# Performance work log

Hardware: AMD Instinct MI355X
Metric: run time of the kernel (lower is better)

The kernel has to match this reference:

```python
import jax, jax.numpy as jnp
import numpy as np

B, T, D = 8, 1024, 1024

def setup_inputs() -> dict:
    key = jax.random.key(0)
    ks = jax.random.split(key, 9)
    s = D ** -0.5
    return {
        "x": jax.random.normal(ks[0], (B, T, D), dtype=jnp.float32),
        "w_q": jax.random.normal(ks[1], (D, D), dtype=jnp.float32) * s,
        "b_q": jax.random.normal(ks[2], (D,), dtype=jnp.float32) * 0.02,
        "w_k": jax.random.normal(ks[3], (D, D), dtype=jnp.float32) * s,
        "b_k": jax.random.normal(ks[4], (D,), dtype=jnp.float32) * 0.02,
        "w_v": jax.random.normal(ks[5], (D, D), dtype=jnp.float32) * s,
        "b_v": jax.random.normal(ks[6], (D,), dtype=jnp.float32) * 0.02,
        "w_o": jax.random.normal(ks[7], (D, D), dtype=jnp.float32) * s,
        "b_o": jax.random.normal(ks[8], (D,), dtype=jnp.float32) * 0.02,
    }

def reference(x, w_q, b_q, w_k, b_k, w_v, b_v, w_o, b_o):
    d = x.shape[-1]
    scale = jnp.asarray(d, x.dtype) ** -0.5
    q = jnp.einsum('btd,ed->bte', x, w_q) + b_q  # nn.Linear: x @ W^T + b
    k = jnp.einsum('btd,ed->bte', x, w_k) + b_k
    v = jnp.einsum('btd,ed->bte', x, w_v) + b_v
    t = x.shape[1]
    causal = jnp.tril(jnp.ones((t, t), dtype=bool))  # (T, T)
    scores = jnp.einsum('bqd,bkd->bqk', q, k) * scale
    scores = jnp.where(causal, scores, -jnp.inf)
    attn = jax.nn.softmax(scores, axis=-1)  # max-subtraction folded in
    out = jnp.einsum('bqk,bkd->bqd', attn, v)
    return jnp.einsum('btd,ed->bte', out, w_o) + b_o
```

## Files before the change

### kernel.cpp

```cpp
#include <hip/hip_runtime.h>

typedef unsigned short u16;
typedef __attribute__((ext_vector_type(8))) short short8;
typedef __attribute__((ext_vector_type(4))) float f32x4;


__device__ __forceinline__ u16 f2bf(float f) {
  unsigned u = __builtin_bit_cast(unsigned, f);
  u += 0x7fffu + ((u >> 16) & 1u);
  return (u16)(u >> 16);
}

__device__ __forceinline__ void gload16(const void* g, void* l) {
  __builtin_amdgcn_global_load_lds(
      (const __attribute__((address_space(1))) unsigned*)g,
      (__attribute__((address_space(3))) unsigned*)l, 16, 0, 0);
}


#define PTILE(RB_C, RB_N, DOSTAGE, VM, LAST)                                  \
  {                                                                           \
    char* cA = sA0 + cur * 49152;                                             \
                                                       \
    if (DOSTAGE) {                                                            \
      const int ns = (cur + 2 >= 3) ? cur - 1 : cur + 2;                      \
      char* dA = sA0 + ns * 49152;                                            \
      _Pragma("unroll") for (int j = 0; j < 3; ++j) {                         \
        gload16(ga[j], dA + la[j]); ga[j] += 64; }                            \
    }                                                                         \
    _Pragma("unroll") for (int kk = 0; kk < 2; ++kk)                          \
      _Pragma("unroll") for (int i = 0; i < 2; ++i) {                         \
        const int rm = wr + 32 + i * 16 + l16;                                \
        a1f[kk][i] = *(const short8*)(cA + rm * 128 +                         \
            (((kk << 2) + quad) ^ (rm & 7)) * 16);                            \
      }                                                                       \
    asm volatile("s_waitcnt lgkmcnt(4)" ::: "memory");                        \
    __builtin_amdgcn_sched_barrier(0);                                        \
    __builtin_amdgcn_s_setprio(1);                                            \
    _Pragma("unroll") for (int kk = 0; kk < 2; ++kk)                          \
      _Pragma("unroll") for (int i = 0; i < 2; ++i)                           \
        _Pragma("unroll") for (int j = 0; j < 4; ++j)                         \
          acc[i][j] = __builtin_amdgcn_mfma_f32_16x16x32_bf16(                \
              a0f[kk][i], RB_C[kk][j], acc[i][j], 0, 0, 0);                   \
    __builtin_amdgcn_s_setprio(0);                                            \
                                                       \
    if (DOSTAGE) {                                                            \
      const int ns = (cur + 2 >= 3) ? cur - 1 : cur + 2;                      \
      char* dA = sA0 + ns * 49152; char* dB = dA + 32768;                     \
      gload16(ga[3], dA + la[3]); ga[3] += 64;                                \
      _Pragma("unroll") for (int j = 0; j < 2; ++j) {                         \
        gload16(gb[j], dB + lb[j]); gb[j] += 64; }                            \
    }                                                                         \
    if (!(LAST)) {                                                            \
      asm volatile("s_waitcnt vmcnt(" #VM ") lgkmcnt(0)" ::: "memory");       \
      __builtin_amdgcn_s_barrier();                                           \
      asm volatile("" ::: "memory");                                          \
      const int nc = (cur + 1 >= 3) ? 0 : cur + 1;                            \
      char* nA = sA0 + nc * 49152; char* nB = nA + 32768;                     \
      _Pragma("unroll") for (int kk = 0; kk < 2; ++kk)                        \
        _Pragma("unroll") for (int j = 0; j < 4; ++j) {                       \
          const int rn = wc + j * 16 + l16;                                   \
          RB_N[kk][j] = *(const short8*)(nB + rn * 128 +                      \
              (((kk << 2) + quad) ^ (rn & 7)) * 16);                          \
        }                                                                     \
      _Pragma("unroll") for (int kk = 0; kk < 2; ++kk)                        \
        _Pragma("unroll") for (int i = 0; i < 2; ++i) {                       \
          const int rm = wr + i * 16 + l16;                                   \
          a0f[kk][i] = *(const short8*)(nA + rm * 128 +                       \
              (((kk << 2) + quad) ^ (rm & 7)) * 16);                          \
        }                                                                     \
    } else {                                                                  \
      asm volatile("s_waitcnt lgkmcnt(0)" ::: "memory");                      \
    }                                                                         \
    __builtin_amdgcn_sched_barrier(0);                                        \
    __builtin_amdgcn_s_setprio(1);                                            \
    _Pragma("unroll") for (int kk = 0; kk < 2; ++kk)                          \
      _Pragma("unroll") for (int i = 0; i < 2; ++i)                           \
        _Pragma("unroll") for (int j = 0; j < 4; ++j)                         \
          acc[2 + i][j] = __builtin_amdgcn_mfma_f32_16x16x32_bf16(            \
              a1f[kk][i], RB_C[kk][j], acc[2 + i][j], 0, 0, 0);               \
    __builtin_amdgcn_s_setprio(0);                                            \
    cur = (cur + 1 >= 3) ? 0 : cur + 1;                                       \
  }

__device__ __forceinline__ void gemm_256x128(
    const u16* __restrict__ A, const u16* __restrict__ B,
    int m0, int n0, int ntiles, char* smem, f32x4 acc[4][4])
{
  const int tid  = threadIdx.x;
  const int lane = tid & 63;
  const int quad = lane >> 4;
  const int l16  = lane & 15;
  const int wave = tid >> 6;
  const int wr   = (wave >> 1) << 6;
  const int wc   = (wave & 1) << 6;

  const u16* ga[4]; int la[4];
  const u16* gb[2]; int lb[2];
#pragma unroll
  for (int j = 0; j < 4; ++j) {
    const int L = j * 512 + tid;
    const int r = L >> 3;
    const int c = (L & 7) ^ (r & 7);
    la[j] = L * 16;
    ga[j] = A + (size_t)(m0 + r) * 1024 + c * 8;
  }
#pragma unroll
  for (int j = 0; j < 2; ++j) {
    const int L = j * 512 + tid;
    const int r = L >> 3;
    const int c = (L & 7) ^ (r & 7);
    lb[j] = L * 16;
    gb[j] = B + (size_t)(n0 + r) * 1024 + c * 8;
  }
  char* const sA0 = smem;

  short8 bfr0[2][4], bfr1[2][4];
  short8 a0f[2][2], a1f[2][2];

  {
    char* dA = sA0; char* dB = sA0 + 32768;
#pragma unroll
    for (int j = 0; j < 4; ++j) { gload16(ga[j], dA + la[j]); ga[j] += 64; }
#pragma unroll
    for (int j = 0; j < 2; ++j) { gload16(gb[j], dB + lb[j]); gb[j] += 64; }
    dA = sA0 + 49152; dB = dA + 32768;
#pragma unroll
    for (int j = 0; j < 4; ++j) { gload16(ga[j], dA + la[j]); ga[j] += 64; }
#pragma unroll
    for (int j = 0; j < 2; ++j) { gload16(gb[j], dB + lb[j]); gb[j] += 64; }
  }
  asm volatile("s_waitcnt vmcnt(6)" ::: "memory");
  __builtin_amdgcn_s_barrier();
  asm volatile("" ::: "memory");
  {
    char* nA = sA0; char* nB = sA0 + 32768;
#pragma unroll
    for (int kk = 0; kk < 2; ++kk)
#pragma unroll
      for (int j = 0; j < 4; ++j) {
        const int rn = wc + j * 16 + l16;
        bfr0[kk][j] = *(const short8*)(nB + rn * 128 + (((kk << 2) + quad) ^ (rn & 7)) * 16);
      }
#pragma unroll
    for (int kk = 0; kk < 2; ++kk)
#pragma unroll
      for (int i = 0; i < 2; ++i) {
        const int rm = wr + i * 16 + l16;
        a0f[kk][i] = *(const short8*)(nA + rm * 128 + (((kk << 2) + quad) ^ (rm & 7)) * 16);
      }
  }

  int cur = 0;
  const int npair = (ntiles >> 1) - 1;
#pragma unroll 1
  for (int it = 0; it < npair; ++it) {
    PTILE(bfr0, bfr1, true, 6, false);
    PTILE(bfr1, bfr0, true, 6, false);
  }
  PTILE(bfr0, bfr1, false, 0, false);
  PTILE(bfr1, bfr0, false, 0, true);
  __syncthreads();
}

#define ACC_ZERO4(acc) { _Pragma("unroll") for (int i=0;i<4;++i) \
  _Pragma("unroll") for (int j=0;j<4;++j) \
  _Pragma("unroll") for (int r=0;r<4;++r) acc[i][j][r]=0.f; }

__device__ __forceinline__ void store256x128_bf16(
    f32x4 acc[4][4], const float* bias, int n0,
    u16* C, int m0, char* smem)
{
  const int tid = threadIdx.x, lane = tid & 63, wave = tid >> 6;
  const int quad = lane >> 4, l16 = lane & 15;
  const int wr = (wave >> 1) << 6, wc = (wave & 1) << 6;
  u16* t = (u16*)smem;
#pragma unroll
  for (int j = 0; j < 4; ++j) {
    const int nn = wc + j * 16 + l16;
    const float bj = bias[n0 + nn];
#pragma unroll
    for (int i = 0; i < 4; ++i) {
      const int mm = wr + i * 16 + quad * 4;
#pragma unroll
      for (int r = 0; r < 4; ++r)
        t[(mm + r) * 136 + nn] = f2bf(acc[i][j][r] + bj);
    }
  }
  __syncthreads();
#pragma unroll
  for (int it = 0; it < 8; ++it) {
    const int L = it * 512 + tid;
    const int mm = L >> 4, cc = L & 15;
    *(uint4*)(C + (size_t)(m0 + mm) * 1024 + n0 + cc * 8) =
        *(const uint4*)(t + mm * 136 + cc * 8);
  }
}

__global__ __launch_bounds__(256) void cast_inputs(
    const float* __restrict__ x,  const float* __restrict__ wq,
    const float* __restrict__ wk, const float* __restrict__ wv,
    const float* __restrict__ wo,
    u16* xb, u16* wqb, u16* wkb, u16* wvb, u16* wob, float* rsum)
{
  int b = blockIdx.x;
  if (b < 8) {
    float4 z = {0.f, 0.f, 0.f, 0.f};
    *(float4*)(rsum + (b * 256 + threadIdx.x) * 4) = z;
  }
  const float* src; u16* dst; int base;
  if (b < 4096) { src = x; dst = xb; base = b * 2048; }
  else {
    int r = (b - 4096) >> 9, bb = (b - 4096) & 511;
    base = bb * 2048;
    src = (r == 0) ? wq : (r == 1) ? wk : (r == 2) ? wv : wo;
    dst = (r == 0) ? wqb : (r == 1) ? wkb : (r == 2) ? wvb : wob;
  }
  int i0 = base + threadIdx.x * 8;
  float4 f0 = *(const float4*)(src + i0);
  float4 f1 = *(const float4*)(src + i0 + 4);
  short8 o;
  o[0]=(short)f2bf(f0.x); o[1]=(short)f2bf(f0.y); o[2]=(short)f2bf(f0.z); o[3]=(short)f2bf(f0.w);
  o[4]=(short)f2bf(f1.x); o[5]=(short)f2bf(f1.y); o[6]=(short)f2bf(f1.z); o[7]=(short)f2bf(f1.w);
  *(short8*)(dst + i0) = o;
}

__global__ __launch_bounds__(512, 2) void proj_qkv(
    const u16* __restrict__ xb,
    const u16* __restrict__ wqb, const u16* __restrict__ wkb, const u16* __restrict__ wvb,
    const float* __restrict__ bq, const float* __restrict__ bk, const float* __restrict__ bv,
    u16* q, u16* k, u16* vt)
{
  __shared__ char smem[147456];
  const int z = blockIdx.y;
  const u16* W = (z == 0) ? wqb : (z == 1) ? wkb : wvb;
  const float* bias = (z == 0) ? bq : (z == 1) ? bk : bv;
  const int id = blockIdx.x;
  const int m0 = ((id & 7) * 4 + ((id >> 3) & 3)) * 256;
  const int n0 = (id >> 5) * 128;

  f32x4 acc[4][4]; ACC_ZERO4(acc);
  gemm_256x128(xb, W, m0, n0, 16, smem, acc);

  if (z < 2) {
    store256x128_bf16(acc, bias, n0, (z == 0) ? q : k, m0, smem);
  } else {
    const int tid = threadIdx.x, lane = tid & 63, wave = tid >> 6;
    const int quad = lane >> 4, l16 = lane & 15;
    const int wr = (wave >> 1) << 6, wc = (wave & 1) << 6;
    u16* t = (u16*)smem;
#pragma unroll
    for (int j = 0; j < 4; ++j) {
      const int nn = wc + j * 16 + l16;
      const float bj = bias[n0 + nn];
#pragma unroll
      for (int i = 0; i < 4; ++i) {
        const int mm = wr + i * 16 + quad * 4;
#pragma unroll
        for (int r = 0; r < 4; ++r)
          t[nn * 264 + mm + r] = f2bf(acc[i][j][r] + bj);
      }
    }
    __syncthreads();
    const int b = m0 >> 10, t0 = m0 & 1023;
#pragma unroll
    for (int it = 0; it < 8; ++it) {
      const int L = it * 512 + tid;
      const int nn = L >> 5, cc = L & 31;
      *(uint4*)(vt + ((size_t)b << 20) + (size_t)(n0 + nn) * 1024 + t0 + cc * 8) =
          *(const uint4*)(t + nn * 264 + cc * 8);
    }
  }
}

__global__ __launch_bounds__(512, 2) void qk_exp256(
    const u16* __restrict__ q, const u16* __restrict__ k,
    u16* __restrict__ probs, float* __restrict__ rowsum)
{
  __shared__ char smem[147456];
  const int id = blockIdx.x;
  const int b = id / 20;
  const int t = id - b * 20;
  const int qi = (t < 2) ? 0 : (t < 6) ? 1 : (t < 12) ? 2 : 3;
  const int pre = (qi == 0) ? 0 : (qi == 1) ? 2 : (qi == 2) ? 6 : 12;
  const int kt = t - pre;
  const int m0 = qi * 256, n0 = kt * 128;
  const u16* A = q + ((size_t)b << 20);
  const u16* B = k + ((size_t)b << 20);

  f32x4 acc[4][4]; ACC_ZERO4(acc);
  gemm_256x128(A, B, m0, n0, 16, smem, acc);

  const int tid = threadIdx.x, lane = tid & 63, wave = tid >> 6;
  const int quad = lane >> 4, l16 = lane & 15;
  const int wr = (wave >> 1) << 6, wc = (wave & 1) << 6;

  float part[4][4];
#pragma unroll
  for (int i = 0; i < 4; ++i)
#pragma unroll
    for (int r = 0; r < 4; ++r) part[i][r] = 0.f;

  u16* tl = (u16*)smem;
#pragma unroll
  for (int j = 0; j < 4; ++j) {
    const int nn = wc + j * 16 + l16;
#pragma unroll
    for (int i = 0; i < 4; ++i) {
      const int mm = wr + i * 16 + quad * 4;
#pragma unroll
      for (int r = 0; r < 4; ++r) {
        float e = __expf(acc[i][j][r] * 0.03125f);
        if ((n0 + nn) > (m0 + mm + r)) e = 0.f;
        part[i][r] += e;
        tl[(mm + r) * 136 + nn] = f2bf(e);
      }
    }
  }
  float* rs = rowsum + b * 1024 + m0;
#pragma unroll
  for (int i = 0; i < 4; ++i)
#pragma unroll
    for (int r = 0; r < 4; ++r) {
      float v = part[i][r];
      v += __shfl_xor(v, 1); v += __shfl_xor(v, 2);
      v += __shfl_xor(v, 4); v += __shfl_xor(v, 8);
      if (l16 == 0) atomicAdd(rs + wr + i * 16 + quad * 4 + r, v);
    }
  __syncthreads();
  u16* C = probs + ((size_t)b << 20);
#pragma unroll
  for (int it = 0; it < 8; ++it) {
    const int L = it * 512 + tid;
    const int mm = L >> 4, cc = L & 15;
    *(uint4*)(C + (size_t)(m0 + mm) * 1024 + n0 + cc * 8) =
        *(const uint4*)(tl + mm * 136 + cc * 8);
  }
}

__global__ __launch_bounds__(512, 2) void pv256(
    const u16* __restrict__ probs, const u16* __restrict__ vt,
    const float* __restrict__ rowsum, u16* __restrict__ o)
{
  __shared__ char smem[147456];
  const int id = blockIdx.x;
  const int b = id & 7;
  const int u = id >> 3;
  const int qi = 3 - (u & 3);
  const int nb = u >> 2;
  const int m0 = qi * 256, n0 = nb * 128;
  const int nt = (qi + 1) * 4;
  const u16* A = probs + ((size_t)b << 20);
  const u16* B = vt + ((size_t)b << 20);

  f32x4 acc[4][4]; ACC_ZERO4(acc);
  gemm_256x128(A, B, m0, n0, nt, smem, acc);

  const int tid = threadIdx.x, lane = tid & 63, wave = tid >> 6;
  const int quad = lane >> 4, l16 = lane & 15;
  const int wr = (wave >> 1) << 6, wc = (wave & 1) << 6;
  const float* rs = rowsum + b * 1024 + m0;
  u16* tl = (u16*)smem;
#pragma unroll
  for (int i = 0; i < 4; ++i)
#pragma unroll
    for (int r = 0; r < 4; ++r) {
      const int mm = wr + i * 16 + quad * 4 + r;
      const float inv = 1.0f / rs[mm];
#pragma unroll
      for (int j = 0; j < 4; ++j)
        tl[mm * 136 + wc + j * 16 + l16] = f2bf(acc[i][j][r] * inv);
    }
  __syncthreads();
  u16* C = o + ((size_t)b << 20);
#pragma unroll
  for (int it = 0; it < 8; ++it) {
    const int L = it * 512 + tid;
    const int mm = L >> 4, cc = L & 15;
    *(uint4*)(C + (size_t)(m0 + mm) * 1024 + n0 + cc * 8) =
        *(const uint4*)(tl + mm * 136 + cc * 8);
  }
}

__global__ __launch_bounds__(512, 2) void proj_o(
    const u16* __restrict__ ob, const u16* __restrict__ wob,
    const float* __restrict__ bo, float* __restrict__ out)
{
  __shared__ char smem[147456];
  const int id = blockIdx.x;
  const int m0 = ((id & 7) * 4 + ((id >> 3) & 3)) * 256;
  const int n0 = (id >> 5) * 128;
  f32x4 acc[4][4]; ACC_ZERO4(acc);
  gemm_256x128(ob, wob, m0, n0, 16, smem, acc);

  const int tid = threadIdx.x, lane = tid & 63, wave = tid >> 6;
  const int quad = lane >> 4, l16 = lane & 15;
  const int wr = (wave >> 1) << 6, wc = (wave & 1) << 6;
  float* tf = (float*)smem;
#pragma unroll
  for (int j = 0; j < 4; ++j) {
    const int nn = wc + j * 16 + l16;
    const float bj = bo[n0 + nn];
#pragma unroll
    for (int i = 0; i < 4; ++i)
#pragma unroll
      for (int r = 0; r < 4; ++r)
        tf[(wr + i * 16 + quad * 4 + r) * 132 + nn] = acc[i][j][r] + bj;
  }
  __syncthreads();
#pragma unroll
  for (int it = 0; it < 16; ++it) {
    const int L = it * 512 + tid;
    const int mm = L >> 5, cc = L & 31;
    *(float4*)(out + (size_t)(m0 + mm) * 1024 + n0 + cc * 4) =
        *(const float4*)(tf + mm * 132 + cc * 4);
  }
}

extern "C" void kernel_launch(void* const* d_in, const int* in_sizes, int n_in,
                              void* d_out, int out_size, void* d_ws, size_t ws_size,
                              hipStream_t stream) {
  const float* x  = (const float*)d_in[0];
  const float* wq = (const float*)d_in[1];
  const float* bq = (const float*)d_in[2];
  const float* wk = (const float*)d_in[3];
  const float* bk = (const float*)d_in[4];
  const float* wv = (const float*)d_in[5];
  const float* bv = (const float*)d_in[6];
  const float* wo = (const float*)d_in[7];
  const float* bo = (const float*)d_in[8];
  float* out = (float*)d_out;

  char* ws = (char*)d_ws;
  const size_t MB = 1u << 20;
  u16*  xb  = (u16*)(ws);
  u16*  wqb = (u16*)(ws + 16*MB);
  u16*  wkb = (u16*)(ws + 18*MB);
  u16*  wvb = (u16*)(ws + 20*MB);
  u16*  wob = (u16*)(ws + 22*MB);
  u16*  qb  = (u16*)(ws + 24*MB);
  u16*  kb  = (u16*)(ws + 40*MB);
  u16*  vtb = (u16*)(ws + 56*MB);
  u16*  pr  = (u16*)(ws + 72*MB);
  float* rsum = (float*)(ws + 88*MB);

  cast_inputs<<<6144, 256, 0, stream>>>(x, wq, wk, wv, wo, xb, wqb, wkb, wvb, wob, rsum);
  proj_qkv<<<dim3(256, 3), 512, 0, stream>>>(xb, wqb, wkb, wvb, bq, bk, bv, qb, kb, vtb);
  qk_exp256<<<160, 512, 0, stream>>>(qb, kb, pr, rsum);
  pv256<<<256, 512, 0, stream>>>(pr, vtb, rsum, xb );
  proj_o<<<256, 512, 0, stream>>>(xb, wob, bo, out);
}
```

Before: 211.9 us.

## Fuse all stages into one cooperative persistent kernel with grid syncs

Merges the cast, QKV projection, QK-exp, PV and output projection kernels into a single cooperative kernel of 256 blocks separated by grid-wide syncs. The QKV projection loops over the three weights inside each block, and the cast is strided across the persistent grid. This aims to remove per-launch overhead and inter-kernel gaps. In exchange it adds grid barrier costs and fixes parallelism at 256 blocks, leaving some blocks idle in the QK stage.

```diff
diff --git a/kernel.cpp b/kernel.cpp
--- a/kernel.cpp
+++ b/kernel.cpp
@@ -1,4 +1,7 @@
 #include <hip/hip_runtime.h>
+#include <hip/hip_cooperative_groups.h>
+
+namespace cg = cooperative_groups;
 
 typedef unsigned short u16;
 typedef __attribute__((ext_vector_type(8))) short short8;
@@ -16,6 +19,8 @@
       (const __attribute__((address_space(1))) unsigned*)g,
       (__attribute__((address_space(3))) unsigned*)l, 16, 0, 0);
 }
+
+#define MFMA16(a, b, c) __builtin_amdgcn_mfma_f32_16x16x32_bf16(a, b, c, 0, 0, 0)
 
 
 #define PTILE(RB_C, RB_N, DOSTAGE, VM, LAST)                                  \
@@ -40,8 +45,7 @@
     _Pragma("unroll") for (int kk = 0; kk < 2; ++kk)                          \
       _Pragma("unroll") for (int i = 0; i < 2; ++i)                           \
         _Pragma("unroll") for (int j = 0; j < 4; ++j)                         \
-          acc[i][j] = __builtin_amdgcn_mfma_f32_16x16x32_bf16(                \
-              a0f[kk][i], RB_C[kk][j], acc[i][j], 0, 0, 0);                   \
+          acc[i][j] = MFMA16(a0f[kk][i], RB_C[kk][j], acc[i][j]);             \
     __builtin_amdgcn_s_setprio(0);                                            \
                                                        \
     if (DOSTAGE) {                                                            \
@@ -77,8 +81,7 @@
     _Pragma("unroll") for (int kk = 0; kk < 2; ++kk)                          \
       _Pragma("unroll") for (int i = 0; i < 2; ++i)                           \
         _Pragma("unroll") for (int j = 0; j < 4; ++j)                         \
-          acc[2 + i][j] = __builtin_amdgcn_mfma_f32_16x16x32_bf16(            \
-              a1f[kk][i], RB_C[kk][j], acc[2 + i][j], 0, 0, 0);               \
+          acc[2 + i][j] = MFMA16(a1f[kk][i], RB_C[kk][j], acc[2 + i][j]);     \
     __builtin_amdgcn_s_setprio(0);                                            \
     cur = (cur + 1 >= 3) ? 0 : cur + 1;                                       \
   }
@@ -197,223 +200,221 @@
   }
 }
 
-__global__ __launch_bounds__(256) void cast_inputs(
-    const float* __restrict__ x,  const float* __restrict__ wq,
-    const float* __restrict__ wk, const float* __restrict__ wv,
-    const float* __restrict__ wo,
-    u16* xb, u16* wqb, u16* wkb, u16* wvb, u16* wob, float* rsum)
-{
-  int b = blockIdx.x;
-  if (b < 8) {
-    float4 z = {0.f, 0.f, 0.f, 0.f};
-    *(float4*)(rsum + (b * 256 + threadIdx.x) * 4) = z;
-  }
-  const float* src; u16* dst; int base;
-  if (b < 4096) { src = x; dst = xb; base = b * 2048; }
-  else {
-    int r = (b - 4096) >> 9, bb = (b - 4096) & 511;
-    base = bb * 2048;
-    src = (r == 0) ? wq : (r == 1) ? wk : (r == 2) ? wv : wo;
-    dst = (r == 0) ? wqb : (r == 1) ? wkb : (r == 2) ? wvb : wob;
-  }
-  int i0 = base + threadIdx.x * 8;
-  float4 f0 = *(const float4*)(src + i0);
-  float4 f1 = *(const float4*)(src + i0 + 4);
-  short8 o;
-  o[0]=(short)f2bf(f0.x); o[1]=(short)f2bf(f0.y); o[2]=(short)f2bf(f0.z); o[3]=(short)f2bf(f0.w);
-  o[4]=(short)f2bf(f1.x); o[5]=(short)f2bf(f1.y); o[6]=(short)f2bf(f1.z); o[7]=(short)f2bf(f1.w);
-  *(short8*)(dst + i0) = o;
-}
-
-__global__ __launch_bounds__(512, 2) void proj_qkv(
-    const u16* __restrict__ xb,
-    const u16* __restrict__ wqb, const u16* __restrict__ wkb, const u16* __restrict__ wvb,
-    const float* __restrict__ bq, const float* __restrict__ bk, const float* __restrict__ bv,
-    u16* q, u16* k, u16* vt)
+__global__ __launch_bounds__(512) void fused_all(
+    const float* __restrict__ x,
+    const float* __restrict__ wq, const float* __restrict__ bq,
+    const float* __restrict__ wk, const float* __restrict__ bk,
+    const float* __restrict__ wv, const float* __restrict__ bv,
+    const float* __restrict__ wo, const float* __restrict__ bo,
+    float* __restrict__ out,
+    u16* xb, u16* wqb, u16* wkb, u16* wvb, u16* wob,
+    u16* qb, u16* kb, u16* vtb, u16* pr, float* rsum)
 {
   __shared__ char smem[147456];
-  const int z = blockIdx.y;
-  const u16* W = (z == 0) ? wqb : (z == 1) ? wkb : wvb;
-  const float* bias = (z == 0) ? bq : (z == 1) ? bk : bv;
-  const int id = blockIdx.x;
-  const int m0 = ((id & 7) * 4 + ((id >> 3) & 3)) * 256;
-  const int n0 = (id >> 5) * 128;
-
-  f32x4 acc[4][4]; ACC_ZERO4(acc);
-  gemm_256x128(xb, W, m0, n0, 16, smem, acc);
-
-  if (z < 2) {
-    store256x128_bf16(acc, bias, n0, (z == 0) ? q : k, m0, smem);
-  } else {
-    const int tid = threadIdx.x, lane = tid & 63, wave = tid >> 6;
+  cg::grid_group grid = cg::this_grid();
+  const int bid = blockIdx.x;
+  const int tid = threadIdx.x;
+
+  {
+    if (bid < 8 && tid < 256) {
+      float4 z4 = {0.f, 0.f, 0.f, 0.f};
+      *(float4*)(rsum + (bid * 256 + tid) * 4) = z4;
+    }
+    const int g0 = bid * 512 + tid;
+#pragma unroll
+    for (int it = 0; it < 12; ++it) {
+      const int u = g0 + it * 131072;
+      const float* src; u16* dst; int idx8;
+      if (u < 1048576) { src = x; dst = xb; idx8 = u; }
+      else {
+        const int w = (u - 1048576) >> 17;
+        idx8 = (u - 1048576) & 131071;
+        src = (w == 0) ? wq : (w == 1) ? wk : (w == 2) ? wv : wo;
+        dst = (w == 0) ? wqb : (w == 1) ? wkb : (w == 2) ? wvb : wob;
+      }
+      const int i0 = idx8 * 8;
+      float4 f0 = *(const float4*)(src + i0);
+      float4 f1 = *(const float4*)(src + i0 + 4);
+      short8 o;
+      o[0]=(short)f2bf(f0.x); o[1]=(short)f2bf(f0.y); o[2]=(short)f2bf(f0.z); o[3]=(short)f2bf(f0.w);
+      o[4]=(short)f2bf(f1.x); o[5]=(short)f2bf(f1.y); o[6]=(short)f2bf(f1.z); o[7]=(short)f2bf(f1.w);
+      *(short8*)(dst + i0) = o;
+    }
+  }
+  grid.sync();
+
+  {
+    const int m0 = ((bid & 7) * 4 + ((bid >> 3) & 3)) * 256;
+    const int n0 = (bid >> 5) * 128;
+    const int lane = tid & 63, wave = tid >> 6;
     const int quad = lane >> 4, l16 = lane & 15;
     const int wr = (wave >> 1) << 6, wc = (wave & 1) << 6;
-    u16* t = (u16*)smem;
+#pragma unroll 1
+    for (int z = 0; z < 3; ++z) {
+      const u16* W = (z == 0) ? wqb : (z == 1) ? wkb : wvb;
+      const float* bias = (z == 0) ? bq : (z == 1) ? bk : bv;
+      f32x4 acc[4][4]; ACC_ZERO4(acc);
+      gemm_256x128(xb, W, m0, n0, 16, smem, acc);
+      if (z < 2) {
+        store256x128_bf16(acc, bias, n0, (z == 0) ? qb : kb, m0, smem);
+      } else {
+        u16* t = (u16*)smem;
+#pragma unroll
+        for (int j = 0; j < 4; ++j) {
+          const int nn = wc + j * 16 + l16;
+          const float bj = bias[n0 + nn];
+#pragma unroll
+          for (int i = 0; i < 4; ++i) {
+            const int mm = wr + i * 16 + quad * 4;
+#pragma unroll
+            for (int r = 0; r < 4; ++r)
+              t[nn * 264 + mm + r] = f2bf(acc[i][j][r] + bj);
+          }
+        }
+        __syncthreads();
+        const int b = m0 >> 10, t0 = m0 & 1023;
+#pragma unroll
+        for (int it = 0; it < 8; ++it) {
+          const int L = it * 512 + tid;
+          const int nn = L >> 5, cc = L & 31;
+          *(uint4*)(vtb + ((size_t)b << 20) + (size_t)(n0 + nn) * 1024 + t0 + cc * 8) =
+              *(const uint4*)(t + nn * 264 + cc * 8);
+        }
+      }
+      __syncthreads();
+    }
+  }
+  grid.sync();
+
+  if (bid < 160) {
+    const int b = bid / 20;
+    const int t = bid - b * 20;
+    const int qi = (t < 2) ? 0 : (t < 6) ? 1 : (t < 12) ? 2 : 3;
+    const int pre = (qi == 0) ? 0 : (qi == 1) ? 2 : (qi == 2) ? 6 : 12;
+    const int kt = t - pre;
+    const int m0 = qi * 256, n0 = kt * 128;
+    const u16* A = qb + ((size_t)b << 20);
+    const u16* B = kb + ((size_t)b << 20);
+
+    f32x4 acc[4][4]; ACC_ZERO4(acc);
+    gemm_256x128(A, B, m0, n0, 16, smem, acc);
+
+    const int lane = tid & 63, wave = tid >> 6;
+    const int quad = lane >> 4, l16 = lane & 15;
+    const int wr = (wave >> 1) << 6, wc = (wave & 1) << 6;
+
+    float part[4][4];
+#pragma unroll
+    for (int i = 0; i < 4; ++i)
+#pragma unroll
+      for (int r = 0; r < 4; ++r) part[i][r] = 0.f;
+
+    u16* tl = (u16*)smem;
 #pragma unroll
     for (int j = 0; j < 4; ++j) {
       const int nn = wc + j * 16 + l16;
-      const float bj = bias[n0 + nn];
 #pragma unroll
       for (int i = 0; i < 4; ++i) {
         const int mm = wr + i * 16 + quad * 4;
 #pragma unroll
-        for (int r = 0; r < 4; ++r)
-          t[nn * 264 + mm + r] = f2bf(acc[i][j][r] + bj);
-      }
-    }
+        for (int r = 0; r < 4; ++r) {
+          float e = __expf(acc[i][j][r] * 0.03125f);
+          if ((n0 + nn) > (m0 + mm + r)) e = 0.f;
+          part[i][r] += e;
+          tl[(mm + r) * 136 + nn] = f2bf(e);
+        }
+      }
+    }
+    float* rs = rsum + b * 1024 + m0;
+#pragma unroll
+    for (int i = 0; i < 4; ++i)
+#pragma unroll
+      for (int r = 0; r < 4; ++r) {
+        float v = part[i][r];
+        v += __shfl_xor(v, 1); v += __shfl_xor(v, 2);
+        v += __shfl_xor(v, 4); v += __shfl_xor(v, 8);
+        if (l16 == 0) atomicAdd(rs + wr + i * 16 + quad * 4 + r, v);
+      }
     __syncthreads();
-    const int b = m0 >> 10, t0 = m0 & 1023;
+    u16* C = pr + ((size_t)b << 20);
 #pragma unroll
     for (int it = 0; it < 8; ++it) {
       const int L = it * 512 + tid;
-      const int nn = L >> 5, cc = L & 31;
-      *(uint4*)(vt + ((size_t)b << 20) + (size_t)(n0 + nn) * 1024 + t0 + cc * 8) =
-          *(const uint4*)(t + nn * 264 + cc * 8);
-    }
-  }
-}
-
-__global__ __launch_bounds__(512, 2) void qk_exp256(
-    const u16* __restrict__ q, const u16* __restrict__ k,
-    u16* __restrict__ probs, float* __restrict__ rowsum)
-{
-  __shared__ char smem[147456];
-  const int id = blockIdx.x;
-  const int b = id / 20;
-  const int t = id - b * 20;
-  const int qi = (t < 2) ? 0 : (t < 6) ? 1 : (t < 12) ? 2 : 3;
-  const int pre = (qi == 0) ? 0 : (qi == 1) ? 2 : (qi == 2) ? 6 : 12;
-  const int kt = t - pre;
-  const int m0 = qi * 256, n0 = kt * 128;
-  const u16* A = q + ((size_t)b << 20);
-  const u16* B = k + ((size_t)b << 20);
-
-  f32x4 acc[4][4]; ACC_ZERO4(acc);
-  gemm_256x128(A, B, m0, n0, 16, smem, acc);
-
-  const int tid = threadIdx.x, lane = tid & 63, wave = tid >> 6;
-  const int quad = lane >> 4, l16 = lane & 15;
-  const int wr = (wave >> 1) << 6, wc = (wave & 1) << 6;
-
-  float part[4][4];
-#pragma unroll
-  for (int i = 0; i < 4; ++i)
-#pragma unroll
-    for (int r = 0; r < 4; ++r) part[i][r] = 0.f;
-
-  u16* tl = (u16*)smem;
-#pragma unroll
-  for (int j = 0; j < 4; ++j) {
-    const int nn = wc + j * 16 + l16;
-#pragma unroll
-    for (int i = 0; i < 4; ++i) {
-      const int mm = wr + i * 16 + quad * 4;
+      const int mm = L >> 4, cc = L & 15;
+      *(uint4*)(C + (size_t)(m0 + mm) * 1024 + n0 + cc * 8) =
+          *(const uint4*)(tl + mm * 136 + cc * 8);
+    }
+  }
+  grid.sync();
+
+  {
+    const int b = bid & 7;
+    const int u = bid >> 3;
+    const int qi = 3 - (u & 3);
+    const int nb = u >> 2;
+    const int m0 = qi * 256, n0 = nb * 128;
+    const int nt = (qi + 1) * 4;
+    const u16* A = pr + ((size_t)b << 20);
+    const u16* B = vtb + ((size_t)b << 20);
+
+    f32x4 acc[4][4]; ACC_ZERO4(acc);
+    gemm_256x128(A, B, m0, n0, nt, smem, acc);
+
+    const int lane = tid & 63, wave = tid >> 6;
+    const int quad = lane >> 4, l16 = lane & 15;
+    const int wr = (wave >> 1) << 6, wc = (wave & 1) << 6;
+    const float* rs = rsum + b * 1024 + m0;
+    u16* tl = (u16*)smem;
+#pragma unroll
+    for (int i = 0; i < 4; ++i)
 #pragma unroll
       for (int r = 0; r < 4; ++r) {
-        float e = __expf(acc[i][j][r] * 0.03125f);
-        if ((n0 + nn) > (m0 + mm + r)) e = 0.f;
-        part[i][r] += e;
-        tl[(mm + r) * 136 + nn] = f2bf(e);
-      }
-    }
-  }
-  float* rs = rowsum + b * 1024 + m0;
-#pragma unroll
-  for (int i = 0; i < 4; ++i)
-#pragma unroll
-    for (int r = 0; r < 4; ++r) {
-      float v = part[i][r];
-      v += __shfl_xor(v, 1); v += __shfl_xor(v, 2);
-      v += __shfl_xor(v, 4); v += __shfl_xor(v, 8);
-      if (l16 == 0) atomicAdd(rs + wr + i * 16 + quad * 4 + r, v);
-    }
-  __syncthreads();
-  u16* C = probs + ((size_t)b << 20);
-#pragma unroll
-  for (int it = 0; it < 8; ++it) {
-    const int L = it * 512 + tid;
-    const int mm = L >> 4, cc = L & 15;
-    *(uint4*)(C + (size_t)(m0 + mm) * 1024 + n0 + cc * 8) =
-        *(const uint4*)(tl + mm * 136 + cc * 8);
-  }
-}
-
-__global__ __launch_bounds__(512, 2) void pv256(
-    const u16* __restrict__ probs, const u16* __restrict__ vt,
-    const float* __restrict__ rowsum, u16* __restrict__ o)
-{
-  __shared__ char smem[147456];
-  const int id = blockIdx.x;
-  const int b = id & 7;
-  const int u = id >> 3;
-  const int qi = 3 - (u & 3);
-  const int nb = u >> 2;
-  const int m0 = qi * 256, n0 = nb * 128;
-  const int nt = (qi + 1) * 4;
-  const u16* A = probs + ((size_t)b << 20);
-  const u16* B = vt + ((size_t)b << 20);
-
-  f32x4 acc[4][4]; ACC_ZERO4(acc);
-  gemm_256x128(A, B, m0, n0, nt, smem, acc);
-
-  const int tid = threadIdx.x, lane = tid & 63, wave = tid >> 6;
-  const int quad = lane >> 4, l16 = lane & 15;
-  const int wr = (wave >> 1) << 6, wc = (wave & 1) << 6;
-  const float* rs = rowsum + b * 1024 + m0;
-  u16* tl = (u16*)smem;
-#pragma unroll
-  for (int i = 0; i < 4; ++i)
-#pragma unroll
-    for (int r = 0; r < 4; ++r) {
-      const int mm = wr + i * 16 + quad * 4 + r;
-      const float inv = 1.0f / rs[mm];
-#pragma unroll
-      for (int j = 0; j < 4; ++j)
-        tl[mm * 136 + wc + j * 16 + l16] = f2bf(acc[i][j][r] * inv);
-    }
-  __syncthreads();
-  u16* C = o + ((size_t)b << 20);
-#pragma unroll
-  for (int it = 0; it < 8; ++it) {
-    const int L = it * 512 + tid;
-    const int mm = L >> 4, cc = L & 15;
-    *(uint4*)(C + (size_t)(m0 + mm) * 1024 + n0 + cc * 8) =
-        *(const uint4*)(tl + mm * 136 + cc * 8);
-  }
-}
-
-__global__ __launch_bounds__(512, 2) void proj_o(
-    const u16* __restrict__ ob, const u16* __restrict__ wob,
-    const float* __restrict__ bo, float* __restrict__ out)
-{
-  __shared__ char smem[147456];
-  const int id = blockIdx.x;
-  const int m0 = ((id & 7) * 4 + ((id >> 3) & 3)) * 256;
-  const int n0 = (id >> 5) * 128;
-  f32x4 acc[4][4]; ACC_ZERO4(acc);
-  gemm_256x128(ob, wob, m0, n0, 16, smem, acc);
-
-  const int tid = threadIdx.x, lane = tid & 63, wave = tid >> 6;
-  const int quad = lane >> 4, l16 = lane & 15;
-  const int wr = (wave >> 1) << 6, wc = (wave & 1) << 6;
-  float* tf = (float*)smem;
-#pragma unroll
-  for (int j = 0; j < 4; ++j) {
-    const int nn = wc + j * 16 + l16;
-    const float bj = bo[n0 + nn];
-#pragma unroll
-    for (int i = 0; i < 4; ++i)
-#pragma unroll
-      for (int r = 0; r < 4; ++r)
-        tf[(wr + i * 16 + quad * 4 + r) * 132 + nn] = acc[i][j][r] + bj;
-  }
-  __syncthreads();
-#pragma unroll
-  for (int it = 0; it < 16; ++it) {
-    const int L = it * 512 + tid;
-    const int mm = L >> 5, cc = L & 31;
-    *(float4*)(out + (size_t)(m0 + mm) * 1024 + n0 + cc * 4) =
-        *(const float4*)(tf + mm * 132 + cc * 4);
+        const int mm = wr + i * 16 + quad * 4 + r;
+        const float inv = 1.0f / rs[mm];
+#pragma unroll
+        for (int j = 0; j < 4; ++j)
+          tl[mm * 136 + wc + j * 16 + l16] = f2bf(acc[i][j][r] * inv);
+      }
+    __syncthreads();
+    u16* C = xb + ((size_t)b << 20);
+#pragma unroll
+    for (int it = 0; it < 8; ++it) {
+      const int L = it * 512 + tid;
+      const int mm = L >> 4, cc = L & 15;
+      *(uint4*)(C + (size_t)(m0 + mm) * 1024 + n0 + cc * 8) =
+          *(const uint4*)(tl + mm * 136 + cc * 8);
+    }
+  }
+  grid.sync();
+
+  {
+    const int m0 = ((bid & 7) * 4 + ((bid >> 3) & 3)) * 256;
+    const int n0 = (bid >> 5) * 128;
+    f32x4 acc[4][4]; ACC_ZERO4(acc);
+    gemm_256x128(xb, wob, m0, n0, 16, smem, acc);
+
+    const int lane = tid & 63, wave = tid >> 6;
+    const int quad = lane >> 4, l16 = lane & 15;
+    const int wr = (wave >> 1) << 6, wc = (wave & 1) << 6;
+    float* tf = (float*)smem;
+#pragma unroll
+    for (int j = 0; j < 4; ++j) {
+      const int nn = wc + j * 16 + l16;
+      const float bj = bo[n0 + nn];
+#pragma unroll
+      for (int i = 0; i < 4; ++i)
+#pragma unroll
+        for (int r = 0; r < 4; ++r)
+          tf[(wr + i * 16 + quad * 4 + r) * 132 + nn] = acc[i][j][r] + bj;
+    }
+    __syncthreads();
+#pragma unroll
+    for (int it = 0; it < 16; ++it) {
+      const int L = it * 512 + tid;
+      const int mm = L >> 5, cc = L & 31;
+      *(float4*)(out + (size_t)(m0 + mm) * 1024 + n0 + cc * 4) =
+          *(const float4*)(tf + mm * 132 + cc * 4);
+    }
   }
 }
 
@@ -444,9 +445,12 @@
   u16*  pr  = (u16*)(ws + 72*MB);
   float* rsum = (float*)(ws + 88*MB);
 
-  cast_inputs<<<6144, 256, 0, stream>>>(x, wq, wk, wv, wo, xb, wqb, wkb, wvb, wob, rsum);
-  proj_qkv<<<dim3(256, 3), 512, 0, stream>>>(xb, wqb, wkb, wvb, bq, bk, bv, qb, kb, vtb);
-  qk_exp256<<<160, 512, 0, stream>>>(qb, kb, pr, rsum);
-  pv256<<<256, 512, 0, stream>>>(pr, vtb, rsum, xb );
-  proj_o<<<256, 512, 0, stream>>>(xb, wob, bo, out);
-}
+  void* args[] = {
+    (void*)&x, (void*)&wq, (void*)&bq, (void*)&wk, (void*)&bk,
+    (void*)&wv, (void*)&bv, (void*)&wo, (void*)&bo, (void*)&out,
+    (void*)&xb, (void*)&wqb, (void*)&wkb, (void*)&wvb, (void*)&wob,
+    (void*)&qb, (void*)&kb, (void*)&vtb, (void*)&pr, (void*)&rsum
+  };
+  hipLaunchCooperativeKernel((const void*)fused_all, dim3(256), dim3(512),
+                             args, 0, stream);
+}
```

After: 391.8 us. 84.9% more time.

## Co-schedule V projection with QK-exp kernel to fill idle CUs

Applied to the files above, without the earlier changes.

The V projection moves out of the QKV projection kernel into a combined launch where blocks 0-159 compute causal QK scores, exp and row sums, and blocks 160-415 compute V^T. The QK kernel alone launched only 160 blocks, which leaves many CUs idle. Running the independent V GEMM in the same grid is meant to fill that gap and remove one launch. In exchange it adds branch divergence at block level, and the scheduling order of the heterogeneous blocks could cause tail imbalance.

```diff
diff --git a/kernel.cpp b/kernel.cpp
--- a/kernel.cpp
+++ b/kernel.cpp
@@ -16,6 +16,8 @@
       (const __attribute__((address_space(1))) unsigned*)g,
       (__attribute__((address_space(3))) unsigned*)l, 16, 0, 0);
 }
+
+#define MFMA16(a, b, c) __builtin_amdgcn_mfma_f32_16x16x32_bf16(a, b, c, 0, 0, 0)
 
 
 #define PTILE(RB_C, RB_N, DOSTAGE, VM, LAST)                                  \
@@ -40,8 +42,7 @@
     _Pragma("unroll") for (int kk = 0; kk < 2; ++kk)                          \
       _Pragma("unroll") for (int i = 0; i < 2; ++i)                           \
         _Pragma("unroll") for (int j = 0; j < 4; ++j)                         \
-          acc[i][j] = __builtin_amdgcn_mfma_f32_16x16x32_bf16(                \
-              a0f[kk][i], RB_C[kk][j], acc[i][j], 0, 0, 0);                   \
+          acc[i][j] = MFMA16(a0f[kk][i], RB_C[kk][j], acc[i][j]);             \
     __builtin_amdgcn_s_setprio(0);                                            \
                                                        \
     if (DOSTAGE) {                                                            \
@@ -77,8 +78,7 @@
     _Pragma("unroll") for (int kk = 0; kk < 2; ++kk)                          \
       _Pragma("unroll") for (int i = 0; i < 2; ++i)                           \
         _Pragma("unroll") for (int j = 0; j < 4; ++j)                         \
-          acc[2 + i][j] = __builtin_amdgcn_mfma_f32_16x16x32_bf16(            \
-              a1f[kk][i], RB_C[kk][j], acc[2 + i][j], 0, 0, 0);               \
+          acc[2 + i][j] = MFMA16(a1f[kk][i], RB_C[kk][j], acc[2 + i][j]);     \
     __builtin_amdgcn_s_setprio(0);                                            \
     cur = (cur + 1 >= 3) ? 0 : cur + 1;                                       \
   }
@@ -225,34 +225,105 @@
   *(short8*)(dst + i0) = o;
 }
 
-__global__ __launch_bounds__(512, 2) void proj_qkv(
+__global__ __launch_bounds__(512, 2) void proj_qk(
     const u16* __restrict__ xb,
-    const u16* __restrict__ wqb, const u16* __restrict__ wkb, const u16* __restrict__ wvb,
-    const float* __restrict__ bq, const float* __restrict__ bk, const float* __restrict__ bv,
-    u16* q, u16* k, u16* vt)
+    const u16* __restrict__ wqb, const u16* __restrict__ wkb,
+    const float* __restrict__ bq, const float* __restrict__ bk,
+    u16* q, u16* k)
 {
   __shared__ char smem[147456];
   const int z = blockIdx.y;
-  const u16* W = (z == 0) ? wqb : (z == 1) ? wkb : wvb;
-  const float* bias = (z == 0) ? bq : (z == 1) ? bk : bv;
+  const u16* W = (z == 0) ? wqb : wkb;
+  const float* bias = (z == 0) ? bq : bk;
   const int id = blockIdx.x;
   const int m0 = ((id & 7) * 4 + ((id >> 3) & 3)) * 256;
   const int n0 = (id >> 5) * 128;
 
   f32x4 acc[4][4]; ACC_ZERO4(acc);
   gemm_256x128(xb, W, m0, n0, 16, smem, acc);
-
-  if (z < 2) {
-    store256x128_bf16(acc, bias, n0, (z == 0) ? q : k, m0, smem);
-  } else {
-    const int tid = threadIdx.x, lane = tid & 63, wave = tid >> 6;
-    const int quad = lane >> 4, l16 = lane & 15;
-    const int wr = (wave >> 1) << 6, wc = (wave & 1) << 6;
-    u16* t = (u16*)smem;
+  store256x128_bf16(acc, bias, n0, (z == 0) ? q : k, m0, smem);
+}
+
+__global__ __launch_bounds__(512, 2) void mix_qk_projv(
+    const u16* __restrict__ qb, const u16* __restrict__ kb,
+    u16* __restrict__ pr, float* __restrict__ rsum,
+    const u16* __restrict__ xb, const u16* __restrict__ wvb,
+    const float* __restrict__ bv, u16* __restrict__ vt)
+{
+  __shared__ char smem[147456];
+  const int bid = blockIdx.x;
+  const int tid = threadIdx.x;
+  const int lane = tid & 63, wave = tid >> 6;
+  const int quad = lane >> 4, l16 = lane & 15;
+  const int wr = (wave >> 1) << 6, wc = (wave & 1) << 6;
+
+  if (bid < 160) {
+    const int b = bid / 20;
+    const int t = bid - b * 20;
+    const int qi = (t < 2) ? 0 : (t < 6) ? 1 : (t < 12) ? 2 : 3;
+    const int pre = (qi == 0) ? 0 : (qi == 1) ? 2 : (qi == 2) ? 6 : 12;
+    const int kt = t - pre;
+    const int m0 = qi * 256, n0 = kt * 128;
+    const u16* A = qb + ((size_t)b << 20);
+    const u16* B = kb + ((size_t)b << 20);
+
+    f32x4 acc[4][4]; ACC_ZERO4(acc);
+    gemm_256x128(A, B, m0, n0, 16, smem, acc);
+
+    float part[4][4];
+#pragma unroll
+    for (int i = 0; i < 4; ++i)
+#pragma unroll
+      for (int r = 0; r < 4; ++r) part[i][r] = 0.f;
+
+    u16* tl = (u16*)smem;
 #pragma unroll
     for (int j = 0; j < 4; ++j) {
       const int nn = wc + j * 16 + l16;
-      const float bj = bias[n0 + nn];
+#pragma unroll
+      for (int i = 0; i < 4; ++i) {
+        const int mm = wr + i * 16 + quad * 4;
+#pragma unroll
+        for (int r = 0; r < 4; ++r) {
+          float e = __expf(acc[i][j][r] * 0.03125f);
+          if ((n0 + nn) > (m0 + mm + r)) e = 0.f;
+          part[i][r] += e;
+          tl[(mm + r) * 136 + nn] = f2bf(e);
+        }
+      }
+    }
+    float* rs = rsum + b * 1024 + m0;
+#pragma unroll
+    for (int i = 0; i < 4; ++i)
+#pragma unroll
+      for (int r = 0; r < 4; ++r) {
+        float v = part[i][r];
+        v += __shfl_xor(v, 1); v += __shfl_xor(v, 2);
+        v += __shfl_xor(v, 4); v += __shfl_xor(v, 8);
+        if (l16 == 0) atomicAdd(rs + wr + i * 16 + quad * 4 + r, v);
+      }
+    __syncthreads();
+    u16* C = pr + ((size_t)b << 20);
+#pragma unroll
+    for (int it = 0; it < 8; ++it) {
+      const int L = it * 512 + tid;
+      const int mm = L >> 4, cc = L & 15;
+      *(uint4*)(C + (size_t)(m0 + mm) * 1024 + n0 + cc * 8) =
+          *(const uint4*)(tl + mm * 136 + cc * 8);
+    }
+  } else {
+    const int id = bid - 160;
+    const int m0 = ((id & 7) * 4 + ((id >> 3) & 3)) * 256;
+    const int n0 = (id >> 5) * 128;
+
+    f32x4 acc[4][4]; ACC_ZERO4(acc);
+    gemm_256x128(xb, wvb, m0, n0, 16, smem, acc);
+
+    u16* t = (u16*)smem;
+#pragma unroll
+    for (int j = 0; j < 4; ++j) {
+      const int nn = wc + j * 16 + l16;
+      const float bj = bv[n0 + nn];
 #pragma unroll
       for (int i = 0; i < 4; ++i) {
         const int mm = wr + i * 16 + quad * 4;
@@ -270,71 +341,6 @@
       *(uint4*)(vt + ((size_t)b << 20) + (size_t)(n0 + nn) * 1024 + t0 + cc * 8) =
           *(const uint4*)(t + nn * 264 + cc * 8);
     }
-  }
-}
-
-__global__ __launch_bounds__(512, 2) void qk_exp256(
-    const u16* __restrict__ q, const u16* __restrict__ k,
-    u16* __restrict__ probs, float* __restrict__ rowsum)
-{
-  __shared__ char smem[147456];
-  const int id = blockIdx.x;
-  const int b = id / 20;
-  const int t = id - b * 20;
-  const int qi = (t < 2) ? 0 : (t < 6) ? 1 : (t < 12) ? 2 : 3;
-  const int pre = (qi == 0) ? 0 : (qi == 1) ? 2 : (qi == 2) ? 6 : 12;
-  const int kt = t - pre;
-  const int m0 = qi * 256, n0 = kt * 128;
-  const u16* A = q + ((size_t)b << 20);
-  const u16* B = k + ((size_t)b << 20);
-
-  f32x4 acc[4][4]; ACC_ZERO4(acc);
-  gemm_256x128(A, B, m0, n0, 16, smem, acc);
-
-  const int tid = threadIdx.x, lane = tid & 63, wave = tid >> 6;
-  const int quad = lane >> 4, l16 = lane & 15;
-  const int wr = (wave >> 1) << 6, wc = (wave & 1) << 6;
-
-  float part[4][4];
-#pragma unroll
-  for (int i = 0; i < 4; ++i)
-#pragma unroll
-    for (int r = 0; r < 4; ++r) part[i][r] = 0.f;
-
-  u16* tl = (u16*)smem;
-#pragma unroll
-  for (int j = 0; j < 4; ++j) {
-    const int nn = wc + j * 16 + l16;
-#pragma unroll
-    for (int i = 0; i < 4; ++i) {
-      const int mm = wr + i * 16 + quad * 4;
-#pragma unroll
-      for (int r = 0; r < 4; ++r) {
-        float e = __expf(acc[i][j][r] * 0.03125f);
-        if ((n0 + nn) > (m0 + mm + r)) e = 0.f;
-        part[i][r] += e;
-        tl[(mm + r) * 136 + nn] = f2bf(e);
-      }
-    }
-  }
-  float* rs = rowsum + b * 1024 + m0;
-#pragma unroll
-  for (int i = 0; i < 4; ++i)
-#pragma unroll
-    for (int r = 0; r < 4; ++r) {
-      float v = part[i][r];
-      v += __shfl_xor(v, 1); v += __shfl_xor(v, 2);
-      v += __shfl_xor(v, 4); v += __shfl_xor(v, 8);
-      if (l16 == 0) atomicAdd(rs + wr + i * 16 + quad * 4 + r, v);
-    }
-  __syncthreads();
-  u16* C = probs + ((size_t)b << 20);
-#pragma unroll
-  for (int it = 0; it < 8; ++it) {
-    const int L = it * 512 + tid;
-    const int mm = L >> 4, cc = L & 15;
-    *(uint4*)(C + (size_t)(m0 + mm) * 1024 + n0 + cc * 8) =
-        *(const uint4*)(tl + mm * 136 + cc * 8);
   }
 }
 
@@ -445,8 +451,8 @@
   float* rsum = (float*)(ws + 88*MB);
 
   cast_inputs<<<6144, 256, 0, stream>>>(x, wq, wk, wv, wo, xb, wqb, wkb, wvb, wob, rsum);
-  proj_qkv<<<dim3(256, 3), 512, 0, stream>>>(xb, wqb, wkb, wvb, bq, bk, bv, qb, kb, vtb);
-  qk_exp256<<<160, 512, 0, stream>>>(qb, kb, pr, rsum);
+  proj_qk<<<dim3(256, 2), 512, 0, stream>>>(xb, wqb, wkb, bq, bk, qb, kb);
+  mix_qk_projv<<<416, 512, 0, stream>>>(qb, kb, pr, rsum, xb, wvb, bv, vtb);
   pv256<<<256, 512, 0, stream>>>(pr, vtb, rsum, xb );
   proj_o<<<256, 512, 0, stream>>>(xb, wob, bo, out);
 }
```

New measurement: 221.8 us. 1.05x slower.
